# Kernel tuning notes

Measured on AMD Instinct MI355X. Metric: run time of the kernel, lower is better.

Reference implementation:

```python
import jax, jax.numpy as jnp
import numpy as np

N = 50000   # nodes
E = 800000  # edges (before self-loops)
B = 2       # extra batch dim
EPS = 1e-5  # BatchNorm eps


def _glorot(k, fi, fo):
    return jax.random.normal(k, (fi, fo), jnp.float32) * (1.0 / np.sqrt(fi))


def setup_inputs() -> dict:
    key = jax.random.key(0)
    ks = jax.random.split(key, 8)
    x = jax.random.normal(ks[0], (1, B, N, 216), jnp.float32)
    edge_index = jax.random.randint(ks[1], (2, E), 0, N, dtype=jnp.int64)
    return {
        "x": x,
        "W1": _glorot(ks[2], 216, 64), "b1": jnp.zeros((64,), jnp.float32),
        "g1": jnp.ones((64,), jnp.float32), "be1": jnp.zeros((64,), jnp.float32),
        "W2": _glorot(ks[3], 64, 8), "b2": jnp.zeros((8,), jnp.float32),
        "g2": jnp.ones((8,), jnp.float32), "be2": jnp.zeros((8,), jnp.float32),
        "W3": _glorot(ks[4], 8, 3), "b3": jnp.zeros((3,), jnp.float32),
        "edge_index": edge_index,
    }


def _gcn_norm(edge_index, n):
    # add self-loops, symmetric normalization D^-1/2 (A+I) D^-1/2
    loops = jnp.arange(n, dtype=edge_index.dtype)
    row = jnp.concatenate([edge_index[0], loops])
    col = jnp.concatenate([edge_index[1], loops])
    deg = jnp.zeros((n,), jnp.float32).at[col].add(1.0)
    dinv = jnp.where(deg > 0, jax.lax.rsqrt(deg), 0.0)
    norm = dinv[row] * dinv[col]  # [E+N]
    return row, col, norm


def _gcn(x, W, b, row, col, norm):
    # x: [1, B, N, Fin]; transform then propagate along node axis (-2)
    xw = jnp.einsum('ubnf,fo->ubno', x, W)
    msgs = xw[:, :, row, :] * norm[None, None, :, None]     # gather at sources
    out = jnp.zeros_like(xw).at[:, :, col, :].add(msgs)     # scatter to targets
    return out + b


def _bn(h, g, be):
    # h: [B, C, N]; batch statistics over (B, N) per channel (training mode)
    mean = h.mean(axis=(0, 2), keepdims=True)
    var = h.var(axis=(0, 2), keepdims=True)
    return (h - mean) * jax.lax.rsqrt(var + EPS) * g[None, :, None] + be[None, :, None]


def reference(x, W1, b1, g1, be1, W2, b2, g2, be2, W3, b3, edge_index):
    n = x.shape[-2]
    row, col, norm = _gcn_norm(edge_index, n)

    h = jax.nn.relu(_gcn(x, W1, b1, row, col, norm))        # [1,B,N,64]
    h = jnp.swapaxes(h[0], 1, 2)                            # [B,64,N]
    h = _bn(h, g1, be1)
    h = jnp.swapaxes(h, 1, 2)[None]                         # [1,B,N,64]

    x1 = _gcn(h, W2, b2, row, col, norm)                    # [1,B,N,8]
    x2 = jax.nn.relu(x1)
    x2 = jnp.swapaxes(x2[0], 1, 2)                          # [B,8,N]
    x2 = _bn(x2, g2, be2)
    x2 = jnp.swapaxes(x2, 1, 2)[None]                       # [1,B,N,8]

    out = _gcn(x2, W3, b3, row, col, norm)                  # [1,B,N,3]
    return (out, x1)
```

## Files before the change

### kernel.cpp

```cpp
#include <hip/hip_runtime.h>
#include <stdint.h>

#define N_NODES 50000
#define N_EDGES 800000
#define BB 2
#define F0 216
#define ROWS (BB*N_NODES)
#define BN_EPS 1e-5f
#define NSB 49
#define KC 24
#define TM 32


__global__ void k_count(const int* __restrict__ ei, int* __restrict__ cnt) {
    int e = blockIdx.x*blockDim.x + threadIdx.x;
    if (e < N_EDGES) {
        int c = ei[N_EDGES + e];
        atomicAdd(&cnt[c], 1);
    }
}

__global__ void k_scanA(const int* __restrict__ cnt, int* __restrict__ incl, int* __restrict__ part,
                        float* __restrict__ dinv) {
    __shared__ int s[1024];
    int t = threadIdx.x;
    int i = blockIdx.x*1024 + t;
    int c = (i < N_NODES) ? cnt[i] : 0;
    if (i < N_NODES) dinv[i] = rsqrtf((float)(c + 1));
    s[t] = c;
    __syncthreads();
    for (int off=1; off<1024; off<<=1) {
        int a = (t >= off) ? s[t-off] : 0;
        __syncthreads();
        s[t] += a;
        __syncthreads();
    }
    if (i < N_NODES) incl[i] = s[t];
    if (t == 1023) part[blockIdx.x] = s[t];
}

__global__ void k_scanB(int* part) {
    if (threadIdx.x == 0 && blockIdx.x == 0) {
        int run = 0;
        for (int b=0; b<NSB; b++) { int v = part[b]; part[b] = run; run += v; }
    }
}

__global__ void k_scanC(const int* __restrict__ cnt, const int* __restrict__ incl, const int* __restrict__ part,
                        int* __restrict__ offs, int* __restrict__ cursor) {
    int i = blockIdx.x*1024 + threadIdx.x;
    if (i < N_NODES) {
        int inc = part[blockIdx.x] + incl[i];
        int ex = inc - cnt[i];
        offs[i] = ex; cursor[i] = ex;
        if (i == N_NODES-1) offs[N_NODES] = inc;
    }
}

__global__ void k_fill(const int* __restrict__ ei, const float* __restrict__ dinv,
                       int* __restrict__ cursor, int* __restrict__ csr_src, float* __restrict__ csr_w) {
    int e = blockIdx.x*blockDim.x + threadIdx.x;
    if (e < N_EDGES) {
        int r = ei[e];
        int c = ei[N_EDGES + e];
        int slot = atomicAdd(&cursor[c], 1);
        csr_src[slot] = r;
        csr_w[slot]  = dinv[r];
    }
}

__global__ __launch_bounds__(256,4) void k_gemm1(const float* __restrict__ x, const float* __restrict__ W1,
                                                 float* __restrict__ xw) {
    __shared__ float xs[TM*F0];
    int t = threadIdx.x;
    int row0 = blockIdx.x * TM;

    const float4* xg = reinterpret_cast<const float4*>(x + (size_t)row0 * F0);
    float4* xs4 = reinterpret_cast<float4*>(xs);
    #pragma unroll
    for (int i = 0; i < 7; i++) {
        int idx = t + i*256;
        if (idx < (TM*F0)/4) xs4[idx] = xg[idx];
    }
    __syncthreads();

    int o2 = t & 31;
    int rw = t >> 5;
    float acc0[4] = {0.f,0.f,0.f,0.f};
    float acc1[4] = {0.f,0.f,0.f,0.f};

    for (int kc = 0; kc < F0; kc += KC) {
        float wa[KC], wb[KC];
        #pragma unroll
        for (int kk = 0; kk < KC; kk++) {
            wa[kk] = W1[(kc+kk)*64 + o2];
            wb[kk] = W1[(kc+kk)*64 + o2 + 32];
        }
        #pragma unroll
        for (int j = 0; j < 4; j++) {
            const float* xr = xs + (rw*4 + j)*F0 + kc;
            #pragma unroll
            for (int kq = 0; kq < KC/4; kq++) {
                float4 xv = *reinterpret_cast<const float4*>(xr + 4*kq);
                acc0[j] += xv.x*wa[4*kq] + xv.y*wa[4*kq+1] + xv.z*wa[4*kq+2] + xv.w*wa[4*kq+3];
                acc1[j] += xv.x*wb[4*kq] + xv.y*wb[4*kq+1] + xv.z*wb[4*kq+2] + xv.w*wb[4*kq+3];
            }
        }
    }

    #pragma unroll
    for (int j = 0; j < 4; j++) {
        int grow = row0 + rw*4 + j;
        xw[(size_t)grow*64 + o2]      = acc0[j];
        xw[(size_t)grow*64 + o2 + 32] = acc1[j];
    }
}

__global__ __launch_bounds__(256) void k_prop1(const float* __restrict__ xw, const int* __restrict__ offs,
                       const int* __restrict__ csr_src, const float* __restrict__ csr_w,
                       const float* __restrict__ dinv, const float* __restrict__ b1,
                       float* __restrict__ h, float* __restrict__ stat) {
    __shared__ float lsum[64], lsq[64];
    int t = threadIdx.x;
    if (t < 64) { lsum[t]=0.f; lsq[t]=0.f; }
    __syncthreads();
    int f = t & 63;
    int wid = blockIdx.x*4 + (t>>6);
    int nwaves = gridDim.x*4;
    float bias = b1[f];
    float ls=0.f, lq=0.f;
    for (int d = wid; d < N_NODES; d += nwaves) {
        int s0 = offs[d], s1 = offs[d+1];
        float a0=0.f, a1=0.f, p0=0.f, p1=0.f, q0=0.f, q1=0.f, r0=0.f, r1=0.f;
        int e = s0;
        for (; e+8 <= s1; e += 8) {
            int i0=csr_src[e],   i1=csr_src[e+1], i2=csr_src[e+2], i3=csr_src[e+3];
            int i4=csr_src[e+4], i5=csr_src[e+5], i6=csr_src[e+6], i7=csr_src[e+7];
            float w0=csr_w[e],   w1=csr_w[e+1], w2=csr_w[e+2], w3=csr_w[e+3];
            float w4=csr_w[e+4], w5=csr_w[e+5], w6=csr_w[e+6], w7=csr_w[e+7];
            a0 += w0*xw[(size_t)i0*64+f];  a1 += w0*xw[(size_t)(N_NODES+i0)*64+f];
            p0 += w1*xw[(size_t)i1*64+f];  p1 += w1*xw[(size_t)(N_NODES+i1)*64+f];
            q0 += w2*xw[(size_t)i2*64+f];  q1 += w2*xw[(size_t)(N_NODES+i2)*64+f];
            r0 += w3*xw[(size_t)i3*64+f];  r1 += w3*xw[(size_t)(N_NODES+i3)*64+f];
            a0 += w4*xw[(size_t)i4*64+f];  a1 += w4*xw[(size_t)(N_NODES+i4)*64+f];
            p0 += w5*xw[(size_t)i5*64+f];  p1 += w5*xw[(size_t)(N_NODES+i5)*64+f];
            q0 += w6*xw[(size_t)i6*64+f];  q1 += w6*xw[(size_t)(N_NODES+i6)*64+f];
            r0 += w7*xw[(size_t)i7*64+f];  r1 += w7*xw[(size_t)(N_NODES+i7)*64+f];
        }
        for (; e+4 <= s1; e += 4) {
            int i0=csr_src[e], i1=csr_src[e+1], i2=csr_src[e+2], i3=csr_src[e+3];
            float w0=csr_w[e], w1=csr_w[e+1], w2=csr_w[e+2], w3=csr_w[e+3];
            a0 += w0*xw[(size_t)i0*64+f];  a1 += w0*xw[(size_t)(N_NODES+i0)*64+f];
            p0 += w1*xw[(size_t)i1*64+f];  p1 += w1*xw[(size_t)(N_NODES+i1)*64+f];
            q0 += w2*xw[(size_t)i2*64+f];  q1 += w2*xw[(size_t)(N_NODES+i2)*64+f];
            r0 += w3*xw[(size_t)i3*64+f];  r1 += w3*xw[(size_t)(N_NODES+i3)*64+f];
        }
        for (; e < s1; e++) {
            int src = csr_src[e]; float w = csr_w[e];
            a0 += w*xw[(size_t)src*64+f];  a1 += w*xw[(size_t)(N_NODES+src)*64+f];
        }
        a0 += p0 + q0 + r0;
        a1 += p1 + q1 + r1;
        float sd = dinv[d];
        a0 += sd * xw[(size_t)d*64 + f];
        a1 += sd * xw[(size_t)(N_NODES+d)*64 + f];
        float h0 = fmaxf(sd*a0 + bias, 0.f);
        float h1 = fmaxf(sd*a1 + bias, 0.f);
        h[(size_t)d*64 + f] = h0;
        h[(size_t)(N_NODES+d)*64 + f] = h1;
        ls += h0 + h1;
        lq += h0*h0 + h1*h1;
    }
    atomicAdd(&lsum[f], ls);
    atomicAdd(&lsq[f], lq);
    __syncthreads();
    if (t < 64) {
        atomicAdd(&stat[t],     lsum[t]);
        atomicAdd(&stat[64+t],  lsq[t]);
    }
}

__global__ __launch_bounds__(256) void k_bn1_gemm2(const float* __restrict__ h, const float* __restrict__ stat,
                        const float* __restrict__ g, const float* __restrict__ be,
                        const float* __restrict__ W2, float* __restrict__ t2) {
    __shared__ float hs[32][68];
    __shared__ float w2s[64*8];
    __shared__ float scS[64], shS[64];
    int t = threadIdx.x;
    if (t < 64) {
        float inv_n = 1.0f / (float)(BB*N_NODES);
        float mean = stat[t]*inv_n;
        float var  = stat[64+t]*inv_n - mean*mean;
        float is   = rsqrtf(var + BN_EPS);
        float scale = g[t]*is;
        scS[t] = scale;
        shS[t] = be[t] - mean*scale;
    }
    for (int i=t; i<512; i+=256) w2s[i] = W2[i];
    __syncthreads();
    int row0 = blockIdx.x*32;
    for (int idx=t; idx<2048; idx+=256) {
        int r = idx>>6, f = idx&63;
        int grow = row0 + r;
        hs[r][f] = (grow < ROWS) ? h[(size_t)grow*64+f]*scS[f] + shS[f] : 0.f;
    }
    __syncthreads();
    int r = t >> 3, o = t & 7;
    float acc = 0.f;
    #pragma unroll
    for (int f=0; f<64; f++) acc += hs[r][f] * w2s[f*8+o];
    int grow = row0 + r;
    if (grow < ROWS) t2[(size_t)grow*8 + o] = acc;
}

__global__ __launch_bounds__(256) void k_prop2(const float* __restrict__ t2, const int* __restrict__ offs,
                       const int* __restrict__ csr_src, const float* __restrict__ csr_w,
                       const float* __restrict__ dinv, const float* __restrict__ b2,
                       float* __restrict__ x1_out, float* __restrict__ stat) {
    __shared__ float lsum[8], lsq[8];
    int t = threadIdx.x;
    if (t < 8) { lsum[t]=0.f; lsq[t]=0.f; }
    __syncthreads();
    int lane = t & 63;
    int o = lane & 7, b = (lane>>3)&1, es = lane>>4;
    int wid = blockIdx.x*4 + (t>>6);
    int nwaves = gridDim.x*4;
    float bias = b2[o];
    float ls=0.f, lq=0.f;
    for (int d=wid; d<N_NODES; d+=nwaves) {
        int s0=offs[d], s1=offs[d+1];
        float accA=0.f, accB=0.f;
        int e = s0 + es;
        for (; e+4 < s1; e += 8) {
            accA += csr_w[e]   * t2[(size_t)(b*N_NODES+csr_src[e])*8 + o];
            accB += csr_w[e+4] * t2[(size_t)(b*N_NODES+csr_src[e+4])*8 + o];
        }
        if (e < s1) accA += csr_w[e] * t2[(size_t)(b*N_NODES+csr_src[e])*8 + o];
        float acc = accA + accB;
        acc += __shfl_xor(acc, 16, 64);
        acc += __shfl_xor(acc, 32, 64);
        float sd = dinv[d];
        float val = sd*(acc + sd*t2[(size_t)(b*N_NODES+d)*8 + o]) + bias;
        if (es == 0) {
            x1_out[(size_t)(b*N_NODES+d)*8 + o] = val;
            float rv = fmaxf(val, 0.f);
            ls += rv; lq += rv*rv;
        }
    }
    if (es == 0) { atomicAdd(&lsum[o], ls); atomicAdd(&lsq[o], lq); }
    __syncthreads();
    if (t < 8) { atomicAdd(&stat[t], lsum[t]); atomicAdd(&stat[8+t], lsq[t]); }
}

__global__ void k_bn2_gemm3(const float* __restrict__ x1, const float* __restrict__ stat,
                            const float* __restrict__ g, const float* __restrict__ be,
                            const float* __restrict__ W3, float* __restrict__ t3) {
    int rowi = blockIdx.x*blockDim.x + threadIdx.x;
    if (rowi < ROWS) {
        float inv_n = 1.0f / (float)(BB*N_NODES);
        float v[8];
        #pragma unroll
        for (int o=0;o<8;o++) {
            float mean = stat[o]*inv_n;
            float var  = stat[8+o]*inv_n - mean*mean;
            float is   = rsqrtf(var + BN_EPS);
            float scale = g[o]*is;
            float shift = be[o] - mean*scale;
            float r = fmaxf(x1[(size_t)rowi*8+o], 0.f);
            v[o] = r*scale + shift;
        }
        #pragma unroll
        for (int c=0;c<3;c++) {
            float acc=0.f;
            #pragma unroll
            for (int o=0;o<8;o++) acc += v[o]*W3[o*3+c];
            t3[(size_t)rowi*4+c] = acc;
        }
        t3[(size_t)rowi*4+3] = 0.f;
    }
}

__global__ __launch_bounds__(256) void k_prop3(const float* __restrict__ t3, const int* __restrict__ offs,
                       const int* __restrict__ csr_src, const float* __restrict__ csr_w,
                       const float* __restrict__ dinv, const float* __restrict__ b3,
                       float* __restrict__ outp) {
    int t = threadIdx.x;
    int lane = t & 63;
    int c = lane & 3, b = (lane>>2)&1, es = lane>>3;
    int wid = blockIdx.x*4 + (t>>6);
    int nwaves = gridDim.x*4;
    float bias = (c<3) ? b3[c] : 0.f;
    for (int d=wid; d<N_NODES; d+=nwaves) {
        int s0=offs[d], s1=offs[d+1];
        float accA=0.f, accB=0.f;
        int e = s0 + es;
        for (; e+8 < s1; e += 16) {
            accA += csr_w[e]   * t3[(size_t)(b*N_NODES+csr_src[e])*4 + c];
            accB += csr_w[e+8] * t3[(size_t)(b*N_NODES+csr_src[e+8])*4 + c];
        }
        if (e < s1) accA += csr_w[e] * t3[(size_t)(b*N_NODES+csr_src[e])*4 + c];
        float acc = accA + accB;
        acc += __shfl_xor(acc, 8, 64);
        acc += __shfl_xor(acc, 16, 64);
        acc += __shfl_xor(acc, 32, 64);
        float sd = dinv[d];
        float val = sd*(acc + sd*t3[(size_t)(b*N_NODES+d)*4 + c]) + bias;
        if (es == 0 && c < 3) outp[(size_t)(b*N_NODES+d)*3 + c] = val;
    }
}

static inline size_t align256(size_t x){ return (x + 255) & ~(size_t)255; }

extern "C" void kernel_launch(void* const* d_in, const int* in_sizes, int n_in,
                              void* d_out, int out_size, void* d_ws, size_t ws_size,
                              hipStream_t stream) {
    const float* x   = (const float*)d_in[0];
    const float* W1  = (const float*)d_in[1];
    const float* b1  = (const float*)d_in[2];
    const float* g1  = (const float*)d_in[3];
    const float* be1 = (const float*)d_in[4];
    const float* W2  = (const float*)d_in[5];
    const float* b2  = (const float*)d_in[6];
    const float* g2  = (const float*)d_in[7];
    const float* be2 = (const float*)d_in[8];
    const float* W3  = (const float*)d_in[9];
    const float* b3  = (const float*)d_in[10];
    const int*   ei  = (const int*)d_in[11];

    float* outp   = (float*)d_out;
    float* x1_out = (float*)d_out + BB*N_NODES*3;

    char* w = (char*)d_ws;
    size_t off = 0;
    auto alloc = [&](size_t bytes) { void* p = w + off; off = align256(off + bytes); return p; };
    int*   cnt    = (int*)  alloc(N_NODES*4);
    float* stat1  = (float*)alloc(128*4);
    float* stat2  = (float*)alloc(16*4);
    size_t zero_bytes = off;
    float* dinv   = (float*)alloc(N_NODES*4);
    int*   incl   = (int*)  alloc(N_NODES*4);
    int*   part   = (int*)  alloc(64*4);
    int*   offs   = (int*)  alloc((N_NODES+1)*4);
    int*   cursor = (int*)  alloc(N_NODES*4);
    int*   csr_src= (int*)  alloc((size_t)N_EDGES*4);
    float* csr_w  = (float*)alloc((size_t)N_EDGES*4);
    float* xw     = (float*)alloc((size_t)ROWS*64*4);
    float* h      = (float*)alloc((size_t)ROWS*64*4);
    float* t2     = xw;
    float* t3     = h;
    (void)ws_size; (void)in_sizes; (void)n_in; (void)out_size;

    hipMemsetAsync(d_ws, 0, zero_bytes, stream);

    k_count <<<(N_EDGES+255)/256, 256, 0, stream>>>(ei, cnt);
    k_scanA <<<NSB, 1024, 0, stream>>>(cnt, incl, part, dinv);
    k_scanB <<<1, 64, 0, stream>>>(part);
    k_scanC <<<NSB, 1024, 0, stream>>>(cnt, incl, part, offs, cursor);
    k_fill  <<<(N_EDGES+255)/256, 256, 0, stream>>>(ei, dinv, cursor, csr_src, csr_w);

    k_gemm1 <<<ROWS/TM, 256, 0, stream>>>(x, W1, xw);
    k_prop1 <<<4096, 256, 0, stream>>>(xw, offs, csr_src, csr_w, dinv, b1, h, stat1);
    k_bn1_gemm2 <<<(ROWS+31)/32, 256, 0, stream>>>(h, stat1, g1, be1, W2, t2);
    k_prop2 <<<4096, 256, 0, stream>>>(t2, offs, csr_src, csr_w, dinv, b2, x1_out, stat2);
    k_bn2_gemm3 <<<(ROWS+255)/256, 256, 0, stream>>>(x1_out, stat2, g2, be2, W3, t3);
    k_prop3 <<<4096, 256, 0, stream>>>(t3, offs, csr_src, csr_w, dinv, b3, outp);
}
```

Before: 609.7 us.

## Double-buffer W1 loads in gemm1, drop 8-wide prop unroll, halve prop grids

The first GEMM now splits the K dimension into 12-wide chunks and double-buffers the W1 register loads, so the next chunk's weights are fetched while the current chunk is being computed. The 8-edge unrolled loop in prop1 is removed, leaving only the 4-wide and scalar loops, which lowers register pressure but also lowers the number of gathers in flight. All three propagation kernels launch 2048 blocks instead of 4096. The changes are independent of each other and could pull in different directions.

Result: slower. 790.6 us (+29.7%).

```diff
diff --git a/kernel.cpp b/kernel.cpp
--- a/kernel.cpp
+++ b/kernel.cpp
@@ -8,7 +8,7 @@
 #define ROWS (BB*N_NODES)
 #define BN_EPS 1e-5f
 #define NSB 49
-#define KC 24
+#define KC2 12
 #define TM 32
 
 
@@ -88,24 +88,36 @@
     int rw = t >> 5;
     float acc0[4] = {0.f,0.f,0.f,0.f};
     float acc1[4] = {0.f,0.f,0.f,0.f};
-
-    for (int kc = 0; kc < F0; kc += KC) {
-        float wa[KC], wb[KC];
+    float wA0[KC2], wB0[KC2], wA1[KC2], wB1[KC2];
+
+    auto loadW = [&](int c, float (&A)[KC2], float (&Bf)[KC2]) {
+        const float* wp = W1 + (size_t)c*KC2*64 + o2;
         #pragma unroll
-        for (int kk = 0; kk < KC; kk++) {
-            wa[kk] = W1[(kc+kk)*64 + o2];
-            wb[kk] = W1[(kc+kk)*64 + o2 + 32];
-        }
+        for (int kk = 0; kk < KC2; kk++) {
+            A[kk]  = wp[kk*64];
+            Bf[kk] = wp[kk*64 + 32];
+        }
+    };
+    auto comp = [&](int c, const float (&A)[KC2], const float (&Bf)[KC2]) {
         #pragma unroll
         for (int j = 0; j < 4; j++) {
-            const float* xr = xs + (rw*4 + j)*F0 + kc;
+            const float* xr = xs + (rw*4 + j)*F0 + c*KC2;
             #pragma unroll
-            for (int kq = 0; kq < KC/4; kq++) {
+            for (int kq = 0; kq < KC2/4; kq++) {
                 float4 xv = *reinterpret_cast<const float4*>(xr + 4*kq);
-                acc0[j] += xv.x*wa[4*kq] + xv.y*wa[4*kq+1] + xv.z*wa[4*kq+2] + xv.w*wa[4*kq+3];
-                acc1[j] += xv.x*wb[4*kq] + xv.y*wb[4*kq+1] + xv.z*wb[4*kq+2] + xv.w*wb[4*kq+3];
+                acc0[j] += xv.x*A[4*kq]  + xv.y*A[4*kq+1]  + xv.z*A[4*kq+2]  + xv.w*A[4*kq+3];
+                acc1[j] += xv.x*Bf[4*kq] + xv.y*Bf[4*kq+1] + xv.z*Bf[4*kq+2] + xv.w*Bf[4*kq+3];
             }
         }
+    };
+
+    const int NCH = F0/KC2;
+    loadW(0, wA0, wB0);
+    for (int c = 0; c < NCH; c += 2) {
+        if (c+1 < NCH) loadW(c+1, wA1, wB1);
+        comp(c, wA0, wB0);
+        if (c+2 < NCH) loadW(c+2, wA0, wB0);
+        comp(c+1, wA1, wB1);
     }
 
     #pragma unroll
@@ -133,20 +145,6 @@
         int s0 = offs[d], s1 = offs[d+1];
         float a0=0.f, a1=0.f, p0=0.f, p1=0.f, q0=0.f, q1=0.f, r0=0.f, r1=0.f;
         int e = s0;
-        for (; e+8 <= s1; e += 8) {
-            int i0=csr_src[e],   i1=csr_src[e+1], i2=csr_src[e+2], i3=csr_src[e+3];
-            int i4=csr_src[e+4], i5=csr_src[e+5], i6=csr_src[e+6], i7=csr_src[e+7];
-            float w0=csr_w[e],   w1=csr_w[e+1], w2=csr_w[e+2], w3=csr_w[e+3];
-            float w4=csr_w[e+4], w5=csr_w[e+5], w6=csr_w[e+6], w7=csr_w[e+7];
-            a0 += w0*xw[(size_t)i0*64+f];  a1 += w0*xw[(size_t)(N_NODES+i0)*64+f];
-            p0 += w1*xw[(size_t)i1*64+f];  p1 += w1*xw[(size_t)(N_NODES+i1)*64+f];
-            q0 += w2*xw[(size_t)i2*64+f];  q1 += w2*xw[(size_t)(N_NODES+i2)*64+f];
-            r0 += w3*xw[(size_t)i3*64+f];  r1 += w3*xw[(size_t)(N_NODES+i3)*64+f];
-            a0 += w4*xw[(size_t)i4*64+f];  a1 += w4*xw[(size_t)(N_NODES+i4)*64+f];
-            p0 += w5*xw[(size_t)i5*64+f];  p1 += w5*xw[(size_t)(N_NODES+i5)*64+f];
-            q0 += w6*xw[(size_t)i6*64+f];  q1 += w6*xw[(size_t)(N_NODES+i6)*64+f];
-            r0 += w7*xw[(size_t)i7*64+f];  r1 += w7*xw[(size_t)(N_NODES+i7)*64+f];
-        }
         for (; e+4 <= s1; e += 4) {
             int i0=csr_src[e], i1=csr_src[e+1], i2=csr_src[e+2], i3=csr_src[e+3];
             float w0=csr_w[e], w1=csr_w[e+1], w2=csr_w[e+2], w3=csr_w[e+3];
@@ -359,9 +357,9 @@
     k_fill  <<<(N_EDGES+255)/256, 256, 0, stream>>>(ei, dinv, cursor, csr_src, csr_w);
 
     k_gemm1 <<<ROWS/TM, 256, 0, stream>>>(x, W1, xw);
-    k_prop1 <<<4096, 256, 0, stream>>>(xw, offs, csr_src, csr_w, dinv, b1, h, stat1);
+    k_prop1 <<<2048, 256, 0, stream>>>(xw, offs, csr_src, csr_w, dinv, b1, h, stat1);
     k_bn1_gemm2 <<<(ROWS+31)/32, 256, 0, stream>>>(h, stat1, g1, be1, W2, t2);
-    k_prop2 <<<4096, 256, 0, stream>>>(t2, offs, csr_src, csr_w, dinv, b2, x1_out, stat2);
+    k_prop2 <<<2048, 256, 0, stream>>>(t2, offs, csr_src, csr_w, dinv, b2, x1_out, stat2);
     k_bn2_gemm3 <<<(ROWS+255)/256, 256, 0, stream>>>(x1_out, stat2, g2, be2, W3, t3);
-    k_prop3 <<<4096, 256, 0, stream>>>(t3, offs, csr_src, csr_w, dinv, b3, outp);
-}
+    k_prop3 <<<2048, 256, 0, stream>>>(t3, offs, csr_src, csr_w, dinv, b3, outp);
+}
```
